# Kernel optimization log

Hardware: AMD Instinct MI355X
Metric: run time of the kernel (lower is better)

The kernel has to match this reference:

```python
import jax, jax.numpy as jnp
import numpy as np

N = 50000      # nodes
E = 800000     # edges (avg degree 16)
F_IN = 32      # node_feat_dim
D = 128        # hidden_dim
L = 4          # n_layers
H = 8          # n_heads
DK = D // H    # 16
NB = 5         # n_bands
NS = 5         # n_stages
DFF = 4 * D    # ffn hidden


def setup_inputs() -> dict:
    key = jax.random.key(0)
    ks = jax.random.split(key, 24)
    s = 0.02
    inp = {}
    # forward args
    inp['x'] = jax.random.normal(ks[0], (N, F_IN), jnp.float32)
    inp['edge_index'] = jax.random.randint(ks[1], (2, E), 0, N)
    inp['edge_attr'] = jax.random.uniform(ks[2], (E,), jnp.float32)
    inp['band_ids'] = jax.random.randint(ks[3], (E,), 0, NB)
    inp['stage_ids'] = jax.random.randint(ks[4], (N,), 0, NS)
    # learned params (dropout in eval mode -> identity)
    inp['stage_emb'] = jax.random.normal(ks[5], (NS, D), jnp.float32) * s
    inp['in_w'] = jax.random.normal(ks[6], (F_IN, D), jnp.float32) * s
    inp['in_b'] = jnp.zeros((D,), jnp.float32)
    inp['Wq'] = jax.random.normal(ks[7], (L, D, D), jnp.float32) * s
    inp['Wk'] = jax.random.normal(ks[8], (L, D, D), jnp.float32) * s
    inp['Wv'] = jax.random.normal(ks[9], (L, D, D), jnp.float32) * s
    inp['Wo'] = jax.random.normal(ks[10], (L, D, D), jnp.float32) * s
    inp['Wo_b'] = jnp.zeros((L, D), jnp.float32)
    inp['band_bias'] = jax.random.normal(ks[11], (L, NB, H), jnp.float32) * s
    inp['ln1_g'] = jnp.ones((L, D), jnp.float32)
    inp['ln1_b'] = jnp.zeros((L, D), jnp.float32)
    inp['ffn_w1'] = jax.random.normal(ks[12], (L, D, DFF), jnp.float32) * s
    inp['ffn_b1'] = jnp.zeros((L, DFF), jnp.float32)
    inp['ffn_w2'] = jax.random.normal(ks[13], (L, DFF, D), jnp.float32) * s
    inp['ffn_b2'] = jnp.zeros((L, D), jnp.float32)
    inp['ln2_g'] = jnp.ones((L, D), jnp.float32)
    inp['ln2_b'] = jnp.zeros((L, D), jnp.float32)
    inp['out_w'] = jax.random.normal(ks[14], (D, D), jnp.float32) * s
    inp['out_b'] = jnp.zeros((D,), jnp.float32)
    return inp


def _layer_norm(x, g, b, eps=1e-5):
    m = x.mean(-1, keepdims=True)
    v = ((x - m) ** 2).mean(-1, keepdims=True)
    return (x - m) * jax.lax.rsqrt(v + eps) * g + b


def reference(x, edge_index, edge_attr, band_ids, stage_ids, stage_emb,
              in_w, in_b, Wq, Wk, Wv, Wo, Wo_b, band_bias,
              ln1_g, ln1_b, ffn_w1, ffn_b1, ffn_w2, ffn_b2,
              ln2_g, ln2_b, out_w, out_b):
    n = x.shape[0]
    src = edge_index[0]  # message sources (j)
    dst = edge_index[1]  # message targets (i) -> softmax / aggregation index
    scale = 1.0 / np.sqrt(DK).astype(np.float32)

    h = x @ in_w + in_b + stage_emb[stage_ids]  # (N, D)

    for l in range(L):
        Q = (h @ Wq[l]).reshape(n, H, DK)
        K = (h @ Wk[l]).reshape(n, H, DK)
        V = (h @ Wv[l]).reshape(n, H, DK)
        # edge-gather dot-product attention logits + band bias, (E, H)
        attn = jnp.einsum('ehd,ehd->eh', Q[dst], K[src]) * scale
        attn = (attn + band_bias[l][band_ids]) * edge_attr[:, None]
        # segment softmax over edges sharing the same destination node
        mx = jax.ops.segment_max(attn, dst, num_segments=n)  # (N, H)
        ex = jnp.exp(attn - mx[dst])
        sm = jax.ops.segment_sum(ex, dst, num_segments=n)
        a = ex / (sm[dst] + 1e-16)  # (E, H)
        # weighted scatter-add of V_j into destination nodes
        agg = jax.ops.segment_sum(a[:, :, None] * V[src], dst, num_segments=n)
        o = agg.reshape(n, D) @ Wo[l] + Wo_b[l]
        h = _layer_norm(o + h, ln1_g[l], ln1_b[l])  # residual (in_dim == out_dim)
        ff = jax.nn.gelu(h @ ffn_w1[l] + ffn_b1[l], approximate=False) @ ffn_w2[l] + ffn_b2[l]
        h = _layer_norm(h + ff, ln2_g[l], ln2_b[l])

    return h @ out_w + out_b
```

## Files before the change

### kernel.cpp

```cpp
#include <hip/hip_runtime.h>
#include <math.h>

constexpr int N_   = 50000;
constexpr int E_   = 800000;
constexpr int FIN_ = 32;
constexpr int D_   = 128;
constexpr int H_   = 8;
constexpr int NB_  = 5;
constexpr int L_   = 4;
constexpr int DFF_ = 512;

typedef __attribute__((ext_vector_type(8))) short short8;
typedef __attribute__((ext_vector_type(4))) short short4v;
typedef __attribute__((ext_vector_type(4))) float f32x4;
typedef __attribute__((ext_vector_type(2))) float f32x2;

__device__ __forceinline__ short f2bf(float f){
  unsigned u = __float_as_uint(f);
  unsigned r = (u + 0x7FFFu + ((u >> 16) & 1u)) >> 16;
  return (short)r;
}
__device__ __forceinline__ float bf2f(short v){
  return __uint_as_float(((unsigned)(unsigned short)v) << 16);
}
__device__ __forceinline__ float bflo(unsigned u){ return __uint_as_float(u << 16); }
__device__ __forceinline__ float bfhi(unsigned u){ return __uint_as_float(u & 0xffff0000u); }

__device__ __forceinline__ unsigned char f2fp8(float x){
  int p = __builtin_amdgcn_cvt_pk_fp8_f32(x, x, 0, false);
  return (unsigned char)(p & 0xFF);
}

__device__ __forceinline__ float gelu_f(float x){
  float xs = x * 0.70710678118654752f;
  float ax = fabsf(xs);
  float t  = __builtin_amdgcn_rcpf(1.0f + 0.3275911f*ax);
  float y  = t*(0.254829592f + t*(-0.284496736f + t*(1.421413741f +
             t*(-1.453152027f + t*1.061405429f))));
  float e  = exp2f(-ax*ax*1.4426950408889634f);
  float er = 1.0f - y*e;
  er = __uint_as_float((__float_as_uint(er) & 0x7fffffffu) |
                       (__float_as_uint(xs) & 0x80000000u));
  return 0.5f*x*(1.0f + er);
}

__device__ __forceinline__ size_t pfidx(int n, int k, int K){
  return ((size_t)(n >> 4)*(2*K) + (size_t)(k >> 3)*16 + (n & 15))*8 + (k & 7);
}

__global__ __launch_bounds__(256)
void conv_weights(const float* __restrict__ Wq, const float* __restrict__ Wk,
                  const float* __restrict__ Wv, const float* __restrict__ Wo,
                  const float* __restrict__ w1, const float* __restrict__ w2,
                  const float* __restrict__ ow,
                  short* __restrict__ wqkvt, short* __restrict__ wot,
                  short* __restrict__ w1t, short* __restrict__ w2t,
                  short* __restrict__ owt){
  int idx = blockIdx.x * blockDim.x + threadIdx.x;
  if (idx < 3*L_*16384){
    int m = idx / (L_*16384);
    int r = idx % (L_*16384);
    int l = r / 16384, e = r % 16384;
    int k = e >> 7, n = e & 127;
    const float* src = (m == 0) ? Wq : ((m == 1) ? Wk : Wv);
    wqkvt[(size_t)(l*3 + m)*16384 + pfidx(n, k, 128)] = f2bf(src[(size_t)l*16384 + e]);
    return;
  }
  idx -= 3*L_*16384;
  if (idx < L_*16384){
    int l = idx / 16384, e = idx % 16384, k = e >> 7, n = e & 127;
    wot[(size_t)l*16384 + pfidx(n, k, 128)] = f2bf(Wo[idx]);
    return;
  }
  idx -= L_*16384;
  if (idx < L_*D_*DFF_){
    int l = idx / 65536, e = idx % 65536;
    int k = e >> 9, n = e & 511;
    w1t[(size_t)l*65536 + pfidx(n, k, 128)] = f2bf(w1[idx]);
    return;
  }
  idx -= L_*D_*DFF_;
  if (idx < L_*DFF_*D_){
    int l = idx / 65536, e = idx % 65536;
    int k = e >> 7, n = e & 127;
    w2t[(size_t)l*65536 + pfidx(n, k, 512)] = f2bf(w2[idx]);
    return;
  }
  idx -= L_*DFF_*D_;
  if (idx < 16384){
    int k = idx >> 7, n = idx & 127;
    owt[pfidx(n, k, 128)] = f2bf(ow[idx]);
  }
}

__global__ __launch_bounds__(256)
void input_proj(const float* __restrict__ x, const float* __restrict__ in_w,
                const float* __restrict__ in_b, const float* __restrict__ se,
                const int* __restrict__ sid, short* __restrict__ hb){
  int sub = threadIdx.x >> 7, d = threadIdx.x & 127;
  int i = blockIdx.x*2 + sub;
  __shared__ float xs[2][FIN_];
  if (d < FIN_) xs[sub][d] = x[(size_t)i*FIN_ + d];
  __syncthreads();
  float acc = in_b[d] + se[(size_t)sid[i]*D_ + d];
  #pragma unroll 8
  for (int k=0;k<FIN_;k++) acc += xs[sub][k]*in_w[k*D_+d];
  hb[(size_t)i*D_+d] = f2bf(acc);
}

__global__ void k_deg(const int* __restrict__ dst, const int* __restrict__ src,
                      const int* __restrict__ band,
                      int* __restrict__ deg, int* __restrict__ pk){
  int e = blockIdx.x*blockDim.x + threadIdx.x;
  if (e < E_){
    atomicAdd(&deg[dst[e]], 1);
    pk[e] = src[e] | (band[e] << 16);
  }
}

__global__ __launch_bounds__(1024)
void k_scan1(const int* __restrict__ deg, int* __restrict__ rowptr,
             int* __restrict__ bsum){
  __shared__ int sm[1024];
  int b = blockIdx.x, tid = threadIdx.x;
  int i = b*1024 + tid;
  int v = (i < N_) ? deg[i] : 0;
  sm[tid] = v; __syncthreads();
  for (int off=1; off<1024; off<<=1){
    int t = (tid>=off) ? sm[tid-off] : 0;
    __syncthreads();
    sm[tid] += t;
    __syncthreads();
  }
  if (i < N_) rowptr[i+1] = sm[tid];
  if (tid == 1023) bsum[b] = sm[1023];
}

__global__ void k_scan2(int* __restrict__ bsum, int nb){
  int tid = threadIdx.x;
  int v = (tid < nb) ? bsum[tid] : 0;
  for (int off=1; off<64; off<<=1){
    int t = __shfl_up(v, off, 64);
    if (tid >= off) v += t;
  }
  if (tid < nb) bsum[tid] = v;
}

__global__ void k_scan3(int* __restrict__ rowptr, const int* __restrict__ bsum){
  int i = blockIdx.x*blockDim.x + threadIdx.x;
  if (i == 0) rowptr[0] = 0;
  if (i < N_){
    int b = i >> 10;
    if (b > 0) rowptr[i+1] += bsum[b-1];
  }
}

__global__ void k_scatter(const int* __restrict__ dst, const int* __restrict__ rowptr,
                          int* __restrict__ fill, int* __restrict__ eord){
  int e = blockIdx.x*blockDim.x + threadIdx.x;
  if (e < E_){
    int d = dst[e];
    int pos = rowptr[d] + atomicAdd(&fill[d], 1);
    eord[pos] = e;
  }
}

__global__ void k_sortseg(const int* __restrict__ rowptr, int* __restrict__ eord){
  int i = blockIdx.x*blockDim.x + threadIdx.x;
  if (i >= N_) return;
  int b = rowptr[i], t = rowptr[i+1];
  for (int p = b+1; p < t; p++){
    int v = eord[p];
    int q = p-1;
    while (q >= b && eord[q] > v){ eord[q+1] = eord[q]; q--; }
    eord[q+1] = v;
  }
}

__global__ void k_emeta(const int* __restrict__ eord, const int* __restrict__ pk,
                        const float* __restrict__ eattr, int2* __restrict__ em){
  int p = blockIdx.x*blockDim.x + threadIdx.x;
  if (p < E_){
    int e = eord[p];
    em[p] = make_int2(pk[e], __float_as_int(eattr[e]));
  }
}

template<int EPI>
__global__ __launch_bounds__(512, 2)
void gemm128_direct(const short* __restrict__ A, const short* __restrict__ Wt,
                    const float* __restrict__ bias,
                    float* Cf, short* Yb, unsigned char* KV8, int M, long wstride){
  const int tid = threadIdx.x;
  const int by  = blockIdx.y;
  Wt += (size_t)by * wstride;
  const short8* W8 = (const short8*)Wt;
  const int m0 = blockIdx.x * 128;
  const int lane = tid & 63, w = tid >> 6;
  const int wr = w >> 2, wc = w & 3;
  const int lrow = lane & 15, lgrp = lane >> 4;
  f32x4 acc[4][2];
  #pragma unroll
  for (int r=0;r<4;r++){ acc[r][0] = {0.f,0.f,0.f,0.f}; acc[r][1] = {0.f,0.f,0.f,0.f}; }
  int rowA[4];
  #pragma unroll
  for (int r=0;r<4;r++){
    int rr = m0 + wr*64 + r*16 + lrow;
    rowA[r] = (rr < M) ? rr : (M-1);
  }
  #pragma unroll
  for (int kk = 0; kk < 4; kk++){
    const int koff = kk*32 + lgrp*8;
    short8 af[4], bfr[2];
    #pragma unroll
    for (int r = 0; r < 4; r++)
      af[r] = *(const short8*)(A + (size_t)rowA[r]*128 + koff);
    #pragma unroll
    for (int c = 0; c < 2; c++)
      bfr[c] = W8[(size_t)(wc*2 + c)*256 + kk*64 + lane];
    #pragma unroll
    for (int r = 0; r < 4; r++)
      #pragma unroll
      for (int c = 0; c < 2; c++)
        acc[r][c] = __builtin_amdgcn_mfma_f32_16x16x32_bf16(af[r], bfr[c], acc[r][c], 0, 0, 0);
  }
  #pragma unroll
  for (int r = 0; r < 4; r++){
    #pragma unroll
    for (int c = 0; c < 2; c++){
      int col = wc*32 + c*16 + lrow;
      float bv = (EPI == 3) ? bias[col] : 0.f;
      #pragma unroll
      for (int v = 0; v < 4; v++){
        int row = m0 + wr*64 + r*16 + lgrp*4 + v;
        if (row < M){
          float o = acc[r][c][v] + bv;
          if (EPI == 3) Cf[(size_t)row*128 + col] = o;
          else if (by == 0) Yb[(size_t)row*128 + col] = f2bf(o);
          else KV8[(size_t)row*256 + (by-1)*128 + col] = f2fp8(o);
        }
      }
    }
  }
}

__global__ __launch_bounds__(256, 4)
void wo_ffn_fused(const short* __restrict__ aggb, const short* __restrict__ wot,
                  const float* __restrict__ wo_b, short* __restrict__ hb,
                  const short* __restrict__ w1t, const float* __restrict__ b1,
                  const short* __restrict__ w2t, const float* __restrict__ b2,
                  const float* __restrict__ g1, const float* __restrict__ bl1,
                  const float* __restrict__ g2, const float* __restrict__ bl2,
                  int M){
  __shared__ char ytile[8192];
  __shared__ char hidb[8192];
  __shared__ float rsum[4][32];
  __shared__ float rsq[4][32];
  const int tid = threadIdx.x;
  const int m0 = blockIdx.x * 32;
  const int lane = tid & 63, w = tid >> 6;
  const int lrow = lane & 15, lgrp = lane >> 4;
  int rowA[2];
  #pragma unroll
  for (int r=0;r<2;r++){
    int rr = m0 + r*16 + lrow;
    rowA[r] = (rr < M) ? rr : (M-1);
  }

  {
    const short8* W8 = (const short8*)wot;
    f32x4 acc[2][2];
    #pragma unroll
    for (int r=0;r<2;r++){ acc[r][0] = {0.f,0.f,0.f,0.f}; acc[r][1] = {0.f,0.f,0.f,0.f}; }
    #pragma unroll
    for (int kk = 0; kk < 4; kk++){
      const int koff = kk*32 + lgrp*8;
      short8 af[2], bfr[2];
      #pragma unroll
      for (int r = 0; r < 2; r++)
        af[r] = *(const short8*)(aggb + (size_t)rowA[r]*128 + koff);
      #pragma unroll
      for (int c = 0; c < 2; c++)
        bfr[c] = W8[(size_t)(w*2 + c)*256 + kk*64 + lane];
      #pragma unroll
      for (int r = 0; r < 2; r++)
        #pragma unroll
        for (int c = 0; c < 2; c++)
          acc[r][c] = __builtin_amdgcn_mfma_f32_16x16x32_bf16(af[r], bfr[c], acc[r][c], 0, 0, 0);
    }
    float o[2][2][4];
    float ps[2][4], pq[2][4];
    #pragma unroll
    for (int r=0;r<2;r++)
      #pragma unroll
      for (int v=0;v<4;v++){ ps[r][v]=0.f; pq[r][v]=0.f; }
    #pragma unroll
    for (int r = 0; r < 2; r++){
      #pragma unroll
      for (int c = 0; c < 2; c++){
        int col = w*32 + c*16 + lrow;
        float bv = wo_b[col];
        #pragma unroll
        for (int v = 0; v < 4; v++){
          int grow = m0 + r*16 + lgrp*4 + v;
          int gr = (grow < M) ? grow : (M-1);
          float oo = acc[r][c][v] + bv + bf2f(hb[(size_t)gr*128 + col]);
          o[r][c][v] = oo;
          ps[r][v] += oo;
          pq[r][v] += oo*oo;
        }
      }
    }
    #pragma unroll
    for (int r = 0; r < 2; r++)
      #pragma unroll
      for (int v = 0; v < 4; v++){
        #pragma unroll
        for (int off = 1; off < 16; off <<= 1){
          ps[r][v] += __shfl_xor(ps[r][v], off, 16);
          pq[r][v] += __shfl_xor(pq[r][v], off, 16);
        }
      }
    if (lrow == 0){
      #pragma unroll
      for (int r = 0; r < 2; r++)
        #pragma unroll
        for (int v = 0; v < 4; v++){
          int row = r*16 + lgrp*4 + v;
          rsum[w][row] = ps[r][v];
          rsq[w][row]  = pq[r][v];
        }
    }
    __syncthreads();
    #pragma unroll
    for (int r = 0; r < 2; r++){
      float gv[2], bv2[2];
      #pragma unroll
      for (int c = 0; c < 2; c++){
        int col = w*32 + c*16 + lrow;
        gv[c] = g1[col]; bv2[c] = bl1[col];
      }
      #pragma unroll
      for (int v = 0; v < 4; v++){
        int row = r*16 + lgrp*4 + v;
        float s = (rsum[0][row]+rsum[1][row]) + (rsum[2][row]+rsum[3][row]);
        float q = (rsq[0][row]+rsq[1][row]) + (rsq[2][row]+rsq[3][row]);
        float mean = s * (1.f/128.f);
        float var  = q * (1.f/128.f) - mean*mean;
        float rstd = rsqrtf(var + 1e-5f);
        #pragma unroll
        for (int c = 0; c < 2; c++){
          int col = w*32 + c*16 + lrow;
          float y = (o[r][c][v] - mean)*rstd*gv[c] + bv2[c];
          int off = row*256 + col*2;
          *(short*)(ytile + (off ^ ((row & 7) << 4))) = f2bf(y);
        }
      }
    }
  }
  __syncthreads();

  const short8* W18 = (const short8*)w1t;
  const short8* W28 = (const short8*)w2t;
  f32x4 acc2[2][2];
  #pragma unroll
  for (int r=0;r<2;r++){ acc2[r][0] = {0.f,0.f,0.f,0.f}; acc2[r][1] = {0.f,0.f,0.f,0.f}; }
  #pragma unroll
  for (int chunk = 0; chunk < 4; chunk++){
    f32x4 acc1[2][2];
    #pragma unroll
    for (int r=0;r<2;r++){ acc1[r][0] = {0.f,0.f,0.f,0.f}; acc1[r][1] = {0.f,0.f,0.f,0.f}; }
    #pragma unroll
    for (int kk = 0; kk < 4; kk++){
      const int kbyt = kk*64 + lgrp*16;
      short8 af[2], bfr[2];
      #pragma unroll
      for (int r = 0; r < 2; r++){
        int row = r*16 + lrow;
        af[r] = *(const short8*)(ytile + ((row*256 + kbyt) ^ ((row & 7) << 4)));
      }
      #pragma unroll
      for (int c = 0; c < 2; c++){
        int nb = chunk*8 + w*2 + c;
        bfr[c] = W18[(size_t)nb*256 + kk*64 + lane];
      }
      #pragma unroll
      for (int r = 0; r < 2; r++)
        #pragma unroll
        for (int c = 0; c < 2; c++)
          acc1[r][c] = __builtin_amdgcn_mfma_f32_16x16x32_bf16(af[r], bfr[c], acc1[r][c], 0, 0, 0);
    }
    __syncthreads();
    #pragma unroll
    for (int r = 0; r < 2; r++){
      #pragma unroll
      for (int c = 0; c < 2; c++){
        int lc = w*32 + c*16 + lrow;
        float bv = b1[chunk*128 + lc];
        #pragma unroll
        for (int v = 0; v < 4; v++){
          int row = r*16 + lgrp*4 + v;
          float g = gelu_f(acc1[r][c][v] + bv);
          int off = row*256 + lc*2;
          *(short*)(hidb + (off ^ ((row & 7) << 4))) = f2bf(g);
        }
      }
    }
    __syncthreads();
    #pragma unroll
    for (int kk2 = 0; kk2 < 4; kk2++){
      short8 ah[2], bh[2];
      #pragma unroll
      for (int r = 0; r < 2; r++){
        int row = r*16 + lrow;
        ah[r] = *(const short8*)(hidb + ((row*256 + kk2*64 + lgrp*16) ^ ((row & 7) << 4)));
      }
      #pragma unroll
      for (int c = 0; c < 2; c++){
        int nb = w*2 + c;
        bh[c] = W28[(size_t)nb*1024 + chunk*256 + kk2*64 + lane];
      }
      #pragma unroll
      for (int r = 0; r < 2; r++)
        #pragma unroll
        for (int c = 0; c < 2; c++)
          acc2[r][c] = __builtin_amdgcn_mfma_f32_16x16x32_bf16(ah[r], bh[c], acc2[r][c], 0, 0, 0);
    }
  }

  {
    float o2[2][2][4];
    float ps[2][4], pq[2][4];
    #pragma unroll
    for (int r=0;r<2;r++)
      #pragma unroll
      for (int v=0;v<4;v++){ ps[r][v]=0.f; pq[r][v]=0.f; }
    #pragma unroll
    for (int r = 0; r < 2; r++){
      #pragma unroll
      for (int c = 0; c < 2; c++){
        int col = w*32 + c*16 + lrow;
        float bv = b2[col];
        #pragma unroll
        for (int v = 0; v < 4; v++){
          int row = r*16 + lgrp*4 + v;
          int off = row*256 + col*2;
          float res = bf2f(*(const short*)(ytile + (off ^ ((row & 7) << 4))));
          float oo = acc2[r][c][v] + bv + res;
          o2[r][c][v] = oo;
          ps[r][v] += oo;
          pq[r][v] += oo*oo;
        }
      }
    }
    #pragma unroll
    for (int r = 0; r < 2; r++)
      #pragma unroll
      for (int v = 0; v < 4; v++){
        #pragma unroll
        for (int off = 1; off < 16; off <<= 1){
          ps[r][v] += __shfl_xor(ps[r][v], off, 16);
          pq[r][v] += __shfl_xor(pq[r][v], off, 16);
        }
      }
    __syncthreads();
    if (lrow == 0){
      #pragma unroll
      for (int r = 0; r < 2; r++)
        #pragma unroll
        for (int v = 0; v < 4; v++){
          int row = r*16 + lgrp*4 + v;
          rsum[w][row] = ps[r][v];
          rsq[w][row]  = pq[r][v];
        }
    }
    __syncthreads();
    #pragma unroll
    for (int r = 0; r < 2; r++){
      float gv[2], bv2[2];
      #pragma unroll
      for (int c = 0; c < 2; c++){
        int col = w*32 + c*16 + lrow;
        gv[c] = g2[col]; bv2[c] = bl2[col];
      }
      #pragma unroll
      for (int v = 0; v < 4; v++){
        int row = r*16 + lgrp*4 + v;
        int grow = m0 + row;
        float s = (rsum[0][row]+rsum[1][row]) + (rsum[2][row]+rsum[3][row]);
        float q = (rsq[0][row]+rsq[1][row]) + (rsq[2][row]+rsq[3][row]);
        float mean = s * (1.f/128.f);
        float var  = q * (1.f/128.f) - mean*mean;
        float rstd = rsqrtf(var + 1e-5f);
        if (grow < M){
          #pragma unroll
          for (int c = 0; c < 2; c++){
            int col = w*32 + c*16 + lrow;
            float y = (o2[r][c][v] - mean)*rstd*gv[c] + bv2[c];
            hb[(size_t)grow*128 + col] = f2bf(y);
          }
        }
      }
    }
  }
}

__global__ __launch_bounds__(256, 8)
void attn_fused(const short* __restrict__ Qb, const unsigned char* __restrict__ KV8,
                const int2* __restrict__ em,
                const int* __restrict__ rowptr,
                const float* __restrict__ bb_l, short* __restrict__ aggb){
  const int lane = threadIdx.x & 63;
  const int i = (blockIdx.x << 2) + (threadIdx.x >> 6);
  if (i >= N_) return;
  const int hh = lane >> 3;
  const unsigned qw = ((const unsigned*)Qb)[(size_t)i*64 + lane];
  const float q0 = bflo(qw), q1 = bfhi(qw);
  const int p0 = __builtin_amdgcn_readfirstlane(rowptr[i]);
  const int p1 = __builtin_amdgcn_readfirstlane(rowptr[i+1]);
  constexpr float L2E = 1.442695040888963f;
  float2 outv = {0.f, 0.f};
  if (p0 < p1){
    float s[4]; float2 acc[4];
    #pragma unroll
    for (int c=0;c<4;c++){ s[c]=0.f; acc[c].x=0.f; acc[c].y=0.f; }
    int sj[4], sjN[4];
    float bb[4], ea[4], bbN[4], eaN[4];
    int kw[4], vw[4], kwN[4], vwN[4];

    auto ldmeta = [&](int gb, int* SJ, float* BB, float* EA){
      #pragma unroll
      for (int c = 0; c < 4; c++){
        int idx = gb + c; idx = (idx < p1) ? idx : (p1 - 1);
        int2 m = em[idx];
        unsigned u = (unsigned)__builtin_amdgcn_readfirstlane(m.x);
        SJ[c] = (int)(u & 0xFFFFu);
        BB[c] = bb_l[(u >> 16)*H_ + hh];
        EA[c] = __uint_as_float((unsigned)__builtin_amdgcn_readfirstlane(m.y));
      }
    };

    ldmeta(p0, sj, bb, ea);
    #pragma unroll
    for (int c = 0; c < 4; c++){
      kw[c] = *(const unsigned short*)(KV8 + (size_t)sj[c]*256 + lane*2);
      vw[c] = *(const unsigned short*)(KV8 + (size_t)sj[c]*256 + 128 + lane*2);
    }
    ldmeta(p0 + 4, sjN, bbN, eaN);

    for (int base = p0; base < p1; base += 4){
      #pragma unroll
      for (int c = 0; c < 4; c++){
        kwN[c] = *(const unsigned short*)(KV8 + (size_t)sjN[c]*256 + lane*2);
        vwN[c] = *(const unsigned short*)(KV8 + (size_t)sjN[c]*256 + 128 + lane*2);
      }
      int sj2[4]; float bb2[4], ea2[4];
      ldmeta(base + 8, sj2, bb2, ea2);
      #pragma unroll
      for (int c = 0; c < 4; c++){
        f32x2 kf = __builtin_amdgcn_cvt_pk_f32_fp8(kw[c], false);
        float dot = q0*kf[0] + q1*kf[1];
        dot += __shfl_xor(dot, 1, 8);
        dot += __shfl_xor(dot, 2, 8);
        dot += __shfl_xor(dot, 4, 8);
        float logit = (dot*0.25f + bb[c]) * ea[c];
        logit = fminf(logit, 60.f);
        if (base + c >= p1) logit = -1.0e30f;
        float wgt = exp2f(logit * L2E);
        f32x2 vf = __builtin_amdgcn_cvt_pk_f32_fp8(vw[c], false);
        s[c]     += wgt;
        acc[c].x += wgt*vf[0];
        acc[c].y += wgt*vf[1];
      }
      #pragma unroll
      for (int c = 0; c < 4; c++){
        kw[c]=kwN[c]; vw[c]=vwN[c];
        sj[c]=sjN[c]; bb[c]=bbN[c]; ea[c]=eaN[c];
        sjN[c]=sj2[c]; bbN[c]=bb2[c]; eaN[c]=ea2[c];
      }
    }
    float S = (s[0]+s[1]) + (s[2]+s[3]);
    float Ax = (acc[0].x+acc[1].x) + (acc[2].x+acc[3].x);
    float Ay = (acc[0].y+acc[1].y) + (acc[2].y+acc[3].y);
    float inv = 1.0f / (S + 1e-16f);
    outv.x = Ax * inv;
    outv.y = Ay * inv;
  }
  unsigned lo = (unsigned)(unsigned short)f2bf(outv.x);
  unsigned hi = (unsigned)(unsigned short)f2bf(outv.y);
  ((unsigned*)aggb)[(size_t)i*64 + lane] = lo | (hi << 16);
}

extern "C" void kernel_launch(void* const* d_in, const int* in_sizes, int n_in,
                              void* d_out, int out_size, void* d_ws, size_t ws_size,
                              hipStream_t stream) {
  const float* x         = (const float*)d_in[0];
  const int*   edge_index= (const int*)  d_in[1];
  const float* edge_attr = (const float*)d_in[2];
  const int*   band_ids  = (const int*)  d_in[3];
  const int*   stage_ids = (const int*)  d_in[4];
  const float* stage_emb = (const float*)d_in[5];
  const float* in_w      = (const float*)d_in[6];
  const float* in_b      = (const float*)d_in[7];
  const float* Wq        = (const float*)d_in[8];
  const float* Wk        = (const float*)d_in[9];
  const float* Wv        = (const float*)d_in[10];
  const float* Wo        = (const float*)d_in[11];
  const float* Wo_b      = (const float*)d_in[12];
  const float* band_bias = (const float*)d_in[13];
  const float* ln1_g     = (const float*)d_in[14];
  const float* ln1_b     = (const float*)d_in[15];
  const float* ffn_w1    = (const float*)d_in[16];
  const float* ffn_b1    = (const float*)d_in[17];
  const float* ffn_w2    = (const float*)d_in[18];
  const float* ffn_b2    = (const float*)d_in[19];
  const float* ln2_g     = (const float*)d_in[20];
  const float* ln2_b     = (const float*)d_in[21];
  const float* out_w     = (const float*)d_in[22];
  const float* out_b     = (const float*)d_in[23];
  float* out = (float*)d_out;

  const size_t ND = (size_t)N_*D_;
  float* ws  = (float*)d_ws;
  short* hb   = (short*)ws;
  short* aggb = (short*)(ws + ND);
  short* qb   = (short*)(ws + 2*ND);
  unsigned char* kv8 = (unsigned char*)(ws + 2*ND + ND/2);
  short* wbuf = (short*)(ws + 3*ND + ND/2);
  short* wqkvt = wbuf;
  short* wot   = wbuf + 196608;
  short* w1t   = wbuf + 262144;
  short* w2t   = wbuf + 524288;
  short* owt   = wbuf + 786432;
  int*  ibase = (int*)(ws + 3*ND + ND/2 + 401408);
  int*  deg   = ibase;
  int*  fill  = ibase + N_;
  int*  rowptr= ibase + 2*N_;
  int*  eord  = ibase + 3*N_ + 1;
  int*  bsum  = ibase + 3*N_ + 1 + E_;
  int*  pk    = ibase + 3*N_ + 1 + E_ + 64;
  int2* em    = (int2*)(ibase + 3*N_ + 1 + 2*E_ + 64);

  const int* srcA = edge_index;
  const int* dstA = edge_index + E_;

  hipMemsetAsync(deg, 0, 2ull*N_*sizeof(int), stream);

  conv_weights<<<3136, 256, 0, stream>>>(Wq, Wk, Wv, Wo, ffn_w1, ffn_w2, out_w,
                                         wqkvt, wot, w1t, w2t, owt);
  input_proj<<<N_/2, 256, 0, stream>>>(x, in_w, in_b, stage_emb, stage_ids, hb);

  k_deg   <<<(E_+255)/256, 256, 0, stream>>>(dstA, srcA, band_ids, deg, pk);
  k_scan1 <<<49, 1024, 0, stream>>>(deg, rowptr, bsum);
  k_scan2 <<<1, 64, 0, stream>>>(bsum, 49);
  k_scan3 <<<(N_+255)/256, 256, 0, stream>>>(rowptr, bsum);
  k_scatter<<<(E_+255)/256, 256, 0, stream>>>(dstA, rowptr, fill, eord);
  k_sortseg<<<(N_+255)/256, 256, 0, stream>>>(rowptr, eord);
  k_emeta <<<(E_+255)/256, 256, 0, stream>>>(eord, pk, edge_attr, em);

  const int GB  = (N_ + 127) / 128;
  const int GB3 = (N_ + 31) / 32;
  const int AB  = (N_ + 3) / 4;

  for (int l = 0; l < L_; l++){
    gemm128_direct<4><<<dim3(GB,3), 512, 0, stream>>>(
        hb, wqkvt + (size_t)l*3*16384, nullptr, nullptr, qb, kv8, N_, 16384L);

    attn_fused<<<AB, 256, 0, stream>>>(qb, kv8, em, rowptr,
                                       band_bias + l*NB_*H_, aggb);

    wo_ffn_fused<<<GB3, 256, 0, stream>>>(
        aggb, wot + (size_t)l*16384, Wo_b + l*D_, hb,
        w1t + (size_t)l*65536, ffn_b1 + l*DFF_,
        w2t + (size_t)l*65536, ffn_b2 + l*D_,
        ln1_g + l*D_, ln1_b + l*D_, ln2_g + l*D_, ln2_b + l*D_, N_);
  }

  gemm128_direct<3><<<GB, 512, 0, stream>>>(
      hb, owt, out_b, out, nullptr, nullptr, N_, 0L);
}
```

Measured before the change: 699.9 us.

## Fuse next layer's QKV projection into the Wo+FFN kernel epilogue

```diff
diff --git a/kernel.cpp b/kernel.cpp
--- a/kernel.cpp
+++ b/kernel.cpp
@@ -251,6 +251,8 @@
                   const short* __restrict__ w2t, const float* __restrict__ b2,
                   const float* __restrict__ g1, const float* __restrict__ bl1,
                   const float* __restrict__ g2, const float* __restrict__ bl2,
+                  const short* __restrict__ qkvw,
+                  short* __restrict__ qb, unsigned char* __restrict__ kv8,
                   int M){
   __shared__ char ytile[8192];
   __shared__ char hidb[8192];
@@ -492,12 +494,57 @@
         float mean = s * (1.f/128.f);
         float var  = q * (1.f/128.f) - mean*mean;
         float rstd = rsqrtf(var + 1e-5f);
-        if (grow < M){
+        #pragma unroll
+        for (int c = 0; c < 2; c++){
+          int col = w*32 + c*16 + lrow;
+          float y = (o2[r][c][v] - mean)*rstd*gv[c] + bv2[c];
+          if (grow < M) hb[(size_t)grow*128 + col] = f2bf(y);
+          int off = row*256 + col*2;
+          *(short*)(ytile + (off ^ ((row & 7) << 4))) = f2bf(y);
+        }
+      }
+    }
+  }
+
+  if (qkvw != nullptr){
+    __syncthreads();
+    #pragma unroll
+    for (int m = 0; m < 3; m++){
+      const short8* Wm = (const short8*)(qkvw + (size_t)m*16384);
+      f32x4 accq[2][2];
+      #pragma unroll
+      for (int r=0;r<2;r++){ accq[r][0] = {0.f,0.f,0.f,0.f}; accq[r][1] = {0.f,0.f,0.f,0.f}; }
+      #pragma unroll
+      for (int kk = 0; kk < 4; kk++){
+        const int kbyt = kk*64 + lgrp*16;
+        short8 af[2], bfr[2];
+        #pragma unroll
+        for (int r = 0; r < 2; r++){
+          int row = r*16 + lrow;
+          af[r] = *(const short8*)(ytile + ((row*256 + kbyt) ^ ((row & 7) << 4)));
+        }
+        #pragma unroll
+        for (int c = 0; c < 2; c++)
+          bfr[c] = Wm[(size_t)(w*2 + c)*256 + kk*64 + lane];
+        #pragma unroll
+        for (int r = 0; r < 2; r++)
           #pragma unroll
-          for (int c = 0; c < 2; c++){
-            int col = w*32 + c*16 + lrow;
-            float y = (o2[r][c][v] - mean)*rstd*gv[c] + bv2[c];
-            hb[(size_t)grow*128 + col] = f2bf(y);
+          for (int c = 0; c < 2; c++)
+            accq[r][c] = __builtin_amdgcn_mfma_f32_16x16x32_bf16(af[r], bfr[c], accq[r][c], 0, 0, 0);
+      }
+      #pragma unroll
+      for (int r = 0; r < 2; r++){
+        #pragma unroll
+        for (int c = 0; c < 2; c++){
+          int col = w*32 + c*16 + lrow;
+          #pragma unroll
+          for (int v = 0; v < 4; v++){
+            int grow = m0 + r*16 + lgrp*4 + v;
+            if (grow < M){
+              float o = accq[r][c][v];
+              if (m == 0) qb[(size_t)grow*128 + col] = f2bf(o);
+              else        kv8[(size_t)grow*256 + (m-1)*128 + col] = f2fp8(o);
+            }
           }
         }
       }
@@ -662,18 +709,20 @@
   const int GB3 = (N_ + 31) / 32;
   const int AB  = (N_ + 3) / 4;
 
+  gemm128_direct<4><<<dim3(GB,3), 512, 0, stream>>>(
+      hb, wqkvt, nullptr, nullptr, qb, kv8, N_, 16384L);
+
   for (int l = 0; l < L_; l++){
-    gemm128_direct<4><<<dim3(GB,3), 512, 0, stream>>>(
-        hb, wqkvt + (size_t)l*3*16384, nullptr, nullptr, qb, kv8, N_, 16384L);
-
     attn_fused<<<AB, 256, 0, stream>>>(qb, kv8, em, rowptr,
                                        band_bias + l*NB_*H_, aggb);
 
+    const short* qkvw_next = (l < L_-1) ? (wqkvt + (size_t)(l+1)*3*16384) : nullptr;
     wo_ffn_fused<<<GB3, 256, 0, stream>>>(
         aggb, wot + (size_t)l*16384, Wo_b + l*D_, hb,
         w1t + (size_t)l*65536, ffn_b1 + l*DFF_,
         w2t + (size_t)l*65536, ffn_b2 + l*D_,
-        ln1_g + l*D_, ln1_b + l*D_, ln2_g + l*D_, ln2_b + l*D_, N_);
+        ln1_g + l*D_, ln1_b + l*D_, ln2_g + l*D_, ln2_b + l*D_,
+        qkvw_next, qb, kv8, N_);
   }
 
   gemm128_direct<3><<<GB, 512, 0, stream>>>(
```

Measured after the change: 657.3 us. 6.1% less time.
